# Kernel optimization log

Measured on AMD Instinct MI355X. Metric: run time of the kernel, lower is better.

## Reference

```python
import jax, jax.numpy as jnp
import numpy as np

GROUP = 128  # W4A16 quantization group size along the input (reduction) dim


def dequant(q, s, z):
    """Dequantize int4 weights. q: [out, in] ints in [0,16); s, z: [out, in//GROUP]."""
    out_f, in_f = q.shape
    g = in_f // GROUP
    qf = q.reshape(out_f, g, GROUP).astype(s.dtype)
    w = (qf - z[:, :, None]) * s[:, :, None]
    return w.reshape(out_f, in_f)


def setup_inputs() -> dict:
    key = jax.random.key(0)
    ks = jax.random.split(key, 11)
    H, I = 4096, 11008
    B, S = 4, 2048
    x = jax.random.normal(ks[0], (B, S, H), dtype=jnp.float32)
    qw_gate = jax.random.randint(ks[1], (I, H), 0, 16, dtype=jnp.int32)
    qw_up = jax.random.randint(ks[2], (I, H), 0, 16, dtype=jnp.int32)
    qw_down = jax.random.randint(ks[3], (H, I), 0, 16, dtype=jnp.int32)
    # scales small so dequantized weights have realistic magnitude; zeros in [0,16)
    s_gate = jax.random.uniform(ks[4], (I, H // GROUP), dtype=jnp.float32) * 0.01
    z_gate = jax.random.uniform(ks[5], (I, H // GROUP), dtype=jnp.float32) * 16.0
    s_up = jax.random.uniform(ks[6], (I, H // GROUP), dtype=jnp.float32) * 0.01
    z_up = jax.random.uniform(ks[7], (I, H // GROUP), dtype=jnp.float32) * 16.0
    s_down = jax.random.uniform(ks[8], (H, I // GROUP), dtype=jnp.float32) * 0.01
    z_down = jax.random.uniform(ks[9], (H, I // GROUP), dtype=jnp.float32) * 16.0
    return {
        "x": x,
        "qw_gate": qw_gate, "qw_up": qw_up, "qw_down": qw_down,
        "s_gate": s_gate, "z_gate": z_gate,
        "s_up": s_up, "z_up": z_up,
        "s_down": s_down, "z_down": z_down,
    }


def reference(x, qw_gate, qw_up, qw_down, s_gate, z_gate, s_up, z_up, s_down, z_down):
    # W4A16 SwiGLU MLP: down( silu(gate(x)) * up(x) )
    Wg = dequant(qw_gate, s_gate, z_gate)   # [I, H]
    Wu = dequant(qw_up, s_up, z_up)         # [I, H]
    Wd = dequant(qw_down, s_down, z_down)   # [H, I]
    g = jnp.einsum('bsh,ih->bsi', x, Wg)
    u = jnp.einsum('bsh,ih->bsi', x, Wu)
    h = jax.nn.silu(g) * u
    return jnp.einsum('bsi,hi->bsh', h, Wd)
```

## Files before the change

kernel.cpp:

```cpp
#include <hip/hip_runtime.h>
#include <hip/hip_fp16.h>

typedef __attribute__((ext_vector_type(8))) short s16x8;
typedef __attribute__((ext_vector_type(8))) _Float16 f16x8;
typedef __attribute__((ext_vector_type(4))) float f32x4;

__global__ void cvt_f32_to_f16_kernel(const float* __restrict__ in,
                                      __half* __restrict__ out, long n) {
  long i = (long)blockIdx.x * blockDim.x + threadIdx.x;
  long stride = (long)gridDim.x * blockDim.x;
  const float4* p4 = (const float4*)in;
  for (long j = i; j * 8 < n; j += stride) {
    float4 a = p4[j * 2];
    float4 b = p4[j * 2 + 1];
    union { s16x8 v; __half2 h2[4]; } w;
    w.h2[0] = __floats2half2_rn(a.x, a.y);
    w.h2[1] = __floats2half2_rn(a.z, a.w);
    w.h2[2] = __floats2half2_rn(b.x, b.y);
    w.h2[3] = __floats2half2_rn(b.z, b.w);
    *(s16x8*)(out + j * 8) = w.v;
  }
}

__global__ void pack_kernel(const int* __restrict__ q, uint32_t* __restrict__ p,
                            long n8) {
  long i = (long)blockIdx.x * blockDim.x + threadIdx.x;
  long stride = (long)gridDim.x * blockDim.x;
  for (; i < n8; i += stride) {
    int4 a = ((const int4*)q)[2 * i];
    int4 b = ((const int4*)q)[2 * i + 1];
    uint32_t w = (uint32_t)a.x | ((uint32_t)a.y << 4) | ((uint32_t)a.z << 8) |
                 ((uint32_t)a.w << 12) | ((uint32_t)b.x << 16) |
                 ((uint32_t)b.y << 20) | ((uint32_t)b.z << 24) |
                 ((uint32_t)b.w << 28);
    p[i] = w;
  }
}

__device__ __forceinline__ s16x8 dq_compute(int4 q0, int4 q1, float s, float z) {
  __half hs = __float2half(s);
  __half2 s2 = __halves2half2(hs, hs);
  __half hc = __float2half(-(64.f + z) * s);
  __half2 c2 = __halves2half2(hc, hc);
  uint32_t b0 = 0x54005400u + ((uint32_t)q0.x << 4) + ((uint32_t)q0.y << 20);
  uint32_t b1 = 0x54005400u + ((uint32_t)q0.z << 4) + ((uint32_t)q0.w << 20);
  uint32_t b2 = 0x54005400u + ((uint32_t)q1.x << 4) + ((uint32_t)q1.y << 20);
  uint32_t b3 = 0x54005400u + ((uint32_t)q1.z << 4) + ((uint32_t)q1.w << 20);
  union { s16x8 v; __half2 h2[4]; } w;
  w.h2[0] = __hfma2(*(__half2*)&b0, s2, c2);
  w.h2[1] = __hfma2(*(__half2*)&b1, s2, c2);
  w.h2[2] = __hfma2(*(__half2*)&b2, s2, c2);
  w.h2[3] = __hfma2(*(__half2*)&b3, s2, c2);
  return w.v;
}

__device__ __forceinline__ s16x8 dq8(uint32_t w, __half2 s2, __half2 c2) {
  union { s16x8 v; __half2 h2[4]; } r;
#pragma unroll
  for (int i = 0; i < 4; ++i) {
    uint32_t t = (w >> (8 * i)) & 0xFFu;
    uint32_t b = 0x54005400u + ((t & 15u) << 4) + ((t >> 4) << 20);
    r.h2[i] = __hfma2(*(__half2*)&b, s2, c2);
  }
  return r.v;
}

__device__ __forceinline__ int xcd_swz(int w0, int nwg) {
  const int q = nwg >> 3, r = nwg & 7;
  const int xcd = w0 & 7, idx = w0 >> 3;
  const int base = (xcd < r) ? xcd * (q + 1) : r * (q + 1) + (xcd - r) * q;
  return base + idx;
}

template <int PK>
__global__ __launch_bounds__(512, 2)
void gateup_kernel(const __half* __restrict__ Xh,
                   const int* __restrict__ Qg, const uint32_t* __restrict__ Pg,
                   const int* __restrict__ Qu, const uint32_t* __restrict__ Pu,
                   const float* __restrict__ Sg, const float* __restrict__ Zg,
                   const float* __restrict__ Su, const float* __restrict__ Zu,
                   __half* __restrict__ Pan, int mbs) {
  constexpr int H = 4096, I = 11008, G = 32;
  const int wg = xcd_swz(blockIdx.x, gridDim.x);
  const int mb = wg % mbs;
  const int nb = wg / mbs;
  const int m0 = mb * 256;
  const int n0 = nb * 128;
  const int tid = threadIdx.x;
  const int lane = tid & 63;
  const int wave = tid >> 6;
  const int wm = (wave >> 1) * 64, wn = (wave & 1) * 64;
  const int l15 = lane & 15, lq = lane >> 4;
  const int rsw = (l15 & 7) << 3;

  __shared__ __half As[2][256][64];
  __shared__ __half Bg[2][128][64];
  __shared__ __half Bu[2][128][64];

  f32x4 accg[4][4], accu[4][4];
#pragma unroll
  for (int i = 0; i < 4; ++i)
#pragma unroll
    for (int j = 0; j < 4; ++j) {
      accg[i][j] = {0.f, 0.f, 0.f, 0.f};
      accu[i][j] = {0.f, 0.f, 0.f, 0.f};
    }

  const int arowD = tid >> 3;
  const int acolD = (((tid & 7) ^ ((tid >> 3) & 7)) << 3);
  const int qrow = tid >> 2, qcol0 = (tid & 3) * 16, qsw = (qrow & 7) << 3;
  const int*      qPg = Qg + (size_t)(n0 + qrow) * H + qcol0;
  const int*      qPu = Qu + (size_t)(n0 + qrow) * H + qcol0;
  const uint32_t* pPg = Pg + (size_t)(n0 + qrow) * (H / 8) + (tid & 3) * 2;
  const uint32_t* pPu = Pu + (size_t)(n0 + qrow) * (H / 8) + (tid & 3) * 2;
  const float* sPg = Sg + (size_t)(n0 + qrow) * G;
  const float* zPg = Zg + (size_t)(n0 + qrow) * G;
  const float* sPu = Su + (size_t)(n0 + qrow) * G;
  const float* zPu = Zu + (size_t)(n0 + qrow) * G;

  int4 qG[4], qU[4];
  uint32_t wG0, wG1, wU0, wU1;
  float sG, zG, sU, zU;

#define STAGE_A(buf, kk)                                              \
  {                                                                   \
    const int _k = (kk);                                              \
    _Pragma("unroll")                                                 \
    for (int c = 0; c < 4; ++c) {                                     \
      const __half* src = Xh + (size_t)(m0 + c * 64 + arowD) * H + _k + acolD; \
      __half* dst = &As[buf][0][0] + (size_t)(c * 512 + tid) * 8;     \
      __builtin_amdgcn_global_load_lds((const __attribute__((address_space(1))) void*)src, \
                                       (__attribute__((address_space(3))) void*)dst, 16, 0, 0); \
    }                                                                 \
  }
#define LOAD_Q(kk)                                                    \
  {                                                                   \
    const int _k = (kk);                                              \
    if (PK) {                                                         \
      wG0 = pPg[_k >> 3]; wG1 = pPg[(_k >> 3) + 1];                   \
      wU0 = pPu[_k >> 3]; wU1 = pPu[(_k >> 3) + 1];                   \
    } else {                                                          \
      _Pragma("unroll")                                               \
      for (int i = 0; i < 4; ++i) qG[i] = ((const int4*)(qPg + _k))[i]; \
      _Pragma("unroll")                                               \
      for (int i = 0; i < 4; ++i) qU[i] = ((const int4*)(qPu + _k))[i]; \
    }                                                                 \
    sG = sPg[_k >> 7]; zG = zPg[_k >> 7];                             \
    sU = sPu[_k >> 7]; zU = zPu[_k >> 7];                             \
  }
#define WRITE_B(buf)                                                  \
  {                                                                   \
    if (PK) {                                                         \
      __half h1 = __float2half(sG);                                   \
      __half2 s2 = __halves2half2(h1, h1);                            \
      __half h2 = __float2half(-(64.f + zG) * sG);                    \
      __half2 c2 = __halves2half2(h2, h2);                            \
      *(s16x8*)&Bg[buf][qrow][(qcol0 + 0) ^ qsw] = dq8(wG0, s2, c2);  \
      *(s16x8*)&Bg[buf][qrow][(qcol0 + 8) ^ qsw] = dq8(wG1, s2, c2);  \
      __half h3 = __float2half(sU);                                   \
      __half2 s3 = __halves2half2(h3, h3);                            \
      __half h4 = __float2half(-(64.f + zU) * sU);                    \
      __half2 c3 = __halves2half2(h4, h4);                            \
      *(s16x8*)&Bu[buf][qrow][(qcol0 + 0) ^ qsw] = dq8(wU0, s3, c3);  \
      *(s16x8*)&Bu[buf][qrow][(qcol0 + 8) ^ qsw] = dq8(wU1, s3, c3);  \
    } else {                                                          \
      *(s16x8*)&Bg[buf][qrow][(qcol0 + 0) ^ qsw] = dq_compute(qG[0], qG[1], sG, zG); \
      *(s16x8*)&Bg[buf][qrow][(qcol0 + 8) ^ qsw] = dq_compute(qG[2], qG[3], sG, zG); \
      *(s16x8*)&Bu[buf][qrow][(qcol0 + 0) ^ qsw] = dq_compute(qU[0], qU[1], sU, zU); \
      *(s16x8*)&Bu[buf][qrow][(qcol0 + 8) ^ qsw] = dq_compute(qU[2], qU[3], sU, zU); \
    }                                                                 \
  }
#define MFMA_BUF(buf)                                                 \
  {                                                                   \
    __builtin_amdgcn_s_setprio(1);                                    \
    _Pragma("unroll")                                                 \
    for (int kk = 0; kk < 2; ++kk) {                                  \
      const int cbase = (kk * 32 + lq * 8) ^ rsw;                     \
      f16x8 af[4];                                                    \
      _Pragma("unroll")                                               \
      for (int i = 0; i < 4; ++i)                                     \
        af[i] = *(const f16x8*)&As[buf][wm + i * 16 + l15][cbase];    \
      _Pragma("unroll")                                               \
      for (int j = 0; j < 4; ++j) {                                   \
        f16x8 bg = *(const f16x8*)&Bg[buf][wn + j * 16 + l15][cbase]; \
        f16x8 bu = *(const f16x8*)&Bu[buf][wn + j * 16 + l15][cbase]; \
        _Pragma("unroll")                                             \
        for (int i = 0; i < 4; ++i) {                                 \
          accg[i][j] = __builtin_amdgcn_mfma_f32_16x16x32_f16(af[i], bg, accg[i][j], 0, 0, 0); \
          accu[i][j] = __builtin_amdgcn_mfma_f32_16x16x32_f16(af[i], bu, accu[i][j], 0, 0, 0); \
        }                                                             \
      }                                                               \
    }                                                                 \
    __builtin_amdgcn_s_setprio(0);                                    \
  }

  const int nt = H / 64;
  STAGE_A(0, 0)
  LOAD_Q(0)
  WRITE_B(0)
  __syncthreads();

  int p = 0;
  for (int t = 0; t < nt; ++t) {
    if (t + 1 < nt) {
      STAGE_A(p ^ 1, (t + 1) * 64)
      LOAD_Q((t + 1) * 64)
    }
    MFMA_BUF(p)
    if (t + 1 < nt) WRITE_B(p ^ 1)
    __syncthreads();
    p ^= 1;
  }
#undef STAGE_A
#undef LOAD_Q
#undef WRITE_B
#undef MFMA_BUF

#pragma unroll
  for (int i = 0; i < 4; ++i)
#pragma unroll
    for (int j = 0; j < 4; ++j)
#pragma unroll
      for (int r = 0; r < 4; ++r) {
        const int row = m0 + wm + i * 16 + lq * 4 + r;
        const int col = n0 + wn + j * 16 + l15;
        float g = accg[i][j][r];
        float u = accu[i][j][r];
        float hv = (g / (1.f + __expf(-g))) * u;
        Pan[(size_t)row * I + col] = __float2half(hv);
      }
}

template <int PK>
__global__ __launch_bounds__(512, 2)
void down_kernel(const __half* __restrict__ Hws,
                 const int* __restrict__ Qd, const uint32_t* __restrict__ QdP,
                 const float* __restrict__ Sd, const float* __restrict__ Zd,
                 float* __restrict__ Out, int mbs) {
  constexpr int K = 11008, N = 4096, G = 86;
  const int wg = xcd_swz(blockIdx.x, gridDim.x);
  const int mb = wg % mbs;
  const int nb = wg / mbs;
  const int m0 = mb * 256, n0 = nb * 128;
  const int tid = threadIdx.x;
  const int lane = tid & 63;
  const int wave = tid >> 6;
  const int wm = (wave >> 1) * 64, wn = (wave & 1) * 64;
  const int l15 = lane & 15, lq = lane >> 4;
  const int rsw = (l15 & 7) << 3;

  __shared__ __half As[2][256][64];
  __shared__ __half Bs[2][128][64];

  f32x4 acc[4][4];
#pragma unroll
  for (int i = 0; i < 4; ++i)
#pragma unroll
    for (int j = 0; j < 4; ++j) acc[i][j] = {0.f, 0.f, 0.f, 0.f};

  const int arowD = tid >> 3;
  const int acolD = (((tid & 7) ^ ((tid >> 3) & 7)) << 3);
  const int qrow = tid >> 2, qcol0 = (tid & 3) * 16, qsw = (qrow & 7) << 3;
  const int*      qP  = Qd  + (size_t)(n0 + qrow) * K + qcol0;
  const uint32_t* qPp = QdP + (size_t)(n0 + qrow) * (K / 8) + (tid & 3) * 2;
  const float* sP = Sd + (size_t)(n0 + qrow) * G;
  const float* zP = Zd + (size_t)(n0 + qrow) * G;

  int4 qA[4], qB[4];
  uint32_t wA0, wA1, wB0, wB1;
  float sA, zA, sB, zB;

#define STAGE_A(buf, kk)                                              \
  {                                                                   \
    const int _k = (kk);                                              \
    _Pragma("unroll")                                                 \
    for (int c = 0; c < 4; ++c) {                                     \
      const __half* src = Hws + (size_t)(m0 + c * 64 + arowD) * K + _k + acolD; \
      __half* dst = &As[buf][0][0] + (size_t)(c * 512 + tid) * 8;     \
      __builtin_amdgcn_global_load_lds((const __attribute__((address_space(1))) void*)src, \
                                       (__attribute__((address_space(3))) void*)dst, 16, 0, 0); \
    }                                                                 \
  }
#define LOAD_Q(set, kk)                                               \
  {                                                                   \
    const int _k = (kk);                                              \
    if (PK) {                                                         \
      w##set##0 = qPp[_k >> 3]; w##set##1 = qPp[(_k >> 3) + 1];       \
    } else {                                                          \
      _Pragma("unroll")                                               \
      for (int i = 0; i < 4; ++i) q##set[i] = ((const int4*)(qP + _k))[i]; \
    }                                                                 \
    s##set = sP[_k >> 7]; z##set = zP[_k >> 7];                       \
  }
#define WRITE_B(buf, set)                                             \
  {                                                                   \
    if (PK) {                                                         \
      __half hs = __float2half(s##set);                               \
      __half2 s2 = __halves2half2(hs, hs);                            \
      __half hc = __float2half(-(64.f + z##set) * s##set);            \
      __half2 c2 = __halves2half2(hc, hc);                            \
      *(s16x8*)&Bs[buf][qrow][(qcol0 + 0) ^ qsw] = dq8(w##set##0, s2, c2); \
      *(s16x8*)&Bs[buf][qrow][(qcol0 + 8) ^ qsw] = dq8(w##set##1, s2, c2); \
    } else {                                                          \
      *(s16x8*)&Bs[buf][qrow][(qcol0 + 0) ^ qsw] = dq_compute(q##set[0], q##set[1], s##set, z##set); \
      *(s16x8*)&Bs[buf][qrow][(qcol0 + 8) ^ qsw] = dq_compute(q##set[2], q##set[3], s##set, z##set); \
    }                                                                 \
  }
#define MFMA_BUF(buf)                                                 \
  {                                                                   \
    __builtin_amdgcn_s_setprio(1);                                    \
    _Pragma("unroll")                                                 \
    for (int kk = 0; kk < 2; ++kk) {                                  \
      const int cbase = (kk * 32 + lq * 8) ^ rsw;                     \
      f16x8 af[4];                                                    \
      _Pragma("unroll")                                               \
      for (int i = 0; i < 4; ++i)                                     \
        af[i] = *(const f16x8*)&As[buf][wm + i * 16 + l15][cbase];    \
      _Pragma("unroll")                                               \
      for (int j = 0; j < 4; ++j) {                                   \
        f16x8 bf = *(const f16x8*)&Bs[buf][wn + j * 16 + l15][cbase]; \
        _Pragma("unroll")                                             \
        for (int i = 0; i < 4; ++i)                                   \
          acc[i][j] = __builtin_amdgcn_mfma_f32_16x16x32_f16(af[i], bf, acc[i][j], 0, 0, 0); \
      }                                                               \
    }                                                                 \
    __builtin_amdgcn_s_setprio(0);                                    \
  }

  const int nt = K / 64;
  STAGE_A(0, 0)
  LOAD_Q(A, 0)
  LOAD_Q(B, 64)
  WRITE_B(0, A)
  __syncthreads();

  for (int t = 0; t < nt; t += 2) {
    if (t + 1 < nt) STAGE_A(1, (t + 1) * 64)
    if (t + 2 < nt) LOAD_Q(A, (t + 2) * 64)
    MFMA_BUF(0)
    if (t + 1 < nt) WRITE_B(1, B)
    __syncthreads();
    if (t + 2 < nt) STAGE_A(0, (t + 2) * 64)
    if (t + 3 < nt) LOAD_Q(B, (t + 3) * 64)
    MFMA_BUF(1)
    if (t + 2 < nt) WRITE_B(0, A)
    __syncthreads();
  }
#undef STAGE_A
#undef LOAD_Q
#undef WRITE_B
#undef MFMA_BUF

#pragma unroll
  for (int i = 0; i < 4; ++i)
#pragma unroll
    for (int j = 0; j < 4; ++j)
#pragma unroll
      for (int r = 0; r < 4; ++r) {
        const int row = m0 + wm + i * 16 + lq * 4 + r;
        const int col = n0 + wn + j * 16 + l15;
        Out[(size_t)row * N + col] = acc[i][j][r];
      }
}

extern "C" void kernel_launch(void* const* d_in, const int* in_sizes, int n_in,
                              void* d_out, int out_size, void* d_ws, size_t ws_size,
                              hipStream_t stream) {
  const float* x  = (const float*)d_in[0];
  const int* qg   = (const int*)d_in[1];
  const int* qu   = (const int*)d_in[2];
  const int* qd   = (const int*)d_in[3];
  const float* sg = (const float*)d_in[4];
  const float* zg = (const float*)d_in[5];
  const float* su = (const float*)d_in[6];
  const float* zu = (const float*)d_in[7];
  const float* sd = (const float*)d_in[8];
  const float* zd = (const float*)d_in[9];
  float* out = (float*)d_out;

  const int M = 8192, H = 4096, I = 11008;
  const long N8 = (long)I * H / 8;

  const int PD_MAX = 1375, PU_MAX = 4127;
  uint32_t* Pd = (uint32_t*)d_out;
  uint32_t* Pg = Pd + N8;
  uint32_t* Pu = Pg + N8;

  pack_kernel<<<2048, 256, 0, stream>>>(qd, Pd, N8);
  pack_kernel<<<2048, 256, 0, stream>>>(qg, Pg, N8);
  pack_kernel<<<2048, 256, 0, stream>>>(qu, Pu, N8);

  const size_t per_row = (size_t)(H + I) * 2;
  long mc = (long)(ws_size / per_row);
  mc &= ~255L;
  if (mc > M) mc = M;
  if (mc < 256) mc = 256;
  const int nch = (int)((M + mc - 1) / mc);
  int base = ((M / nch) / 256) * 256;
  if (base < 256) base = 256;
  int rem = M - base * nch;
  const int nplus = rem > 0 ? rem / 256 : 0;

  __half* wsx = (__half*)d_ws;
  const int McMax = base + (nplus > 0 ? 256 : 0);
  __half* wsh = (__half*)((char*)d_ws + (size_t)McMax * H * 2);

  int mbs_arr[64], mb_arr[64];
  {
    int mb = 0;
    for (int c = 0; c < nch; ++c) {
      int r = base + (c < nplus ? 256 : 0);
      mb_arr[c] = mb;
      mbs_arr[c] = r / 256;
      mb += r;
    }
  }

  int W = M;
  for (int c = nch - 1; c >= 0; --c) {
    const int mbase = mb_arr[c];
    const int mbs = mbs_arr[c];
    const int rows = mbs * 256;
    const bool gu_pk = (PU_MAX < W);
    const bool d_pk = (PD_MAX < W) && (PD_MAX < mbase);

    cvt_f32_to_f16_kernel<<<1024, 256, 0, stream>>>(
        x + (size_t)mbase * H, wsx, (long)rows * H);

    if (gu_pk)
      gateup_kernel<1><<<mbs * (I / 128), 512, 0, stream>>>(
          wsx, qg, Pg, qu, Pu, sg, zg, su, zu, wsh, mbs);
    else
      gateup_kernel<0><<<mbs * (I / 128), 512, 0, stream>>>(
          wsx, qg, Pg, qu, Pu, sg, zg, su, zu, wsh, mbs);

    if (d_pk)
      down_kernel<1><<<mbs * (H / 128), 512, 0, stream>>>(
          wsh, qd, Pd, sd, zd, out + (size_t)mbase * H, mbs);
    else
      down_kernel<0><<<mbs * (H / 128), 512, 0, stream>>>(
          wsh, qd, Pd, sd, zd, out + (size_t)mbase * H, mbs);

    W = mbase;
  }
}
```

Measured before the change: 3.383 ms.

## Fuse next-chunk activation conversion into down kernel and split gate/up packing

The fp32-to-fp16 conversion of the next row chunk's activations now runs inside the down-projection kernel. When that kernel has fewer than 256 GEMM blocks, extra blocks are launched to do the conversion, which removes a separate launch per chunk and lets the conversion overlap the down GEMM. Separately, the gate/up kernel now selects packed-int4 versus raw-int32 weight reads for gate and up independently, so gate can use packed weights once its pack region is no longer overwritten. This adds template variants and makes the down kernel write the shared activation workspace, which relies on gateup having finished reading it (guaranteed by stream order).

```diff
diff --git a/kernel.cpp b/kernel.cpp
--- a/kernel.cpp
+++ b/kernel.cpp
@@ -72,7 +72,7 @@
   return base + idx;
 }
 
-template <int PK>
+template <int PKG, int PKU>
 __global__ __launch_bounds__(512, 2)
 void gateup_kernel(const __half* __restrict__ Xh,
                    const int* __restrict__ Qg, const uint32_t* __restrict__ Pg,
@@ -136,12 +136,13 @@
 #define LOAD_Q(kk)                                                    \
   {                                                                   \
     const int _k = (kk);                                              \
-    if (PK) {                                                         \
-      wG0 = pPg[_k >> 3]; wG1 = pPg[(_k >> 3) + 1];                   \
-      wU0 = pPu[_k >> 3]; wU1 = pPu[(_k >> 3) + 1];                   \
-    } else {                                                          \
+    if (PKG) { wG0 = pPg[_k >> 3]; wG1 = pPg[(_k >> 3) + 1]; }        \
+    else {                                                            \
       _Pragma("unroll")                                               \
       for (int i = 0; i < 4; ++i) qG[i] = ((const int4*)(qPg + _k))[i]; \
+    }                                                                 \
+    if (PKU) { wU0 = pPu[_k >> 3]; wU1 = pPu[(_k >> 3) + 1]; }        \
+    else {                                                            \
       _Pragma("unroll")                                               \
       for (int i = 0; i < 4; ++i) qU[i] = ((const int4*)(qPu + _k))[i]; \
     }                                                                 \
@@ -150,13 +151,18 @@
   }
 #define WRITE_B(buf)                                                  \
   {                                                                   \
-    if (PK) {                                                         \
+    if (PKG) {                                                        \
       __half h1 = __float2half(sG);                                   \
       __half2 s2 = __halves2half2(h1, h1);                            \
       __half h2 = __float2half(-(64.f + zG) * sG);                    \
       __half2 c2 = __halves2half2(h2, h2);                            \
       *(s16x8*)&Bg[buf][qrow][(qcol0 + 0) ^ qsw] = dq8(wG0, s2, c2);  \
       *(s16x8*)&Bg[buf][qrow][(qcol0 + 8) ^ qsw] = dq8(wG1, s2, c2);  \
+    } else {                                                          \
+      *(s16x8*)&Bg[buf][qrow][(qcol0 + 0) ^ qsw] = dq_compute(qG[0], qG[1], sG, zG); \
+      *(s16x8*)&Bg[buf][qrow][(qcol0 + 8) ^ qsw] = dq_compute(qG[2], qG[3], sG, zG); \
+    }                                                                 \
+    if (PKU) {                                                        \
       __half h3 = __float2half(sU);                                   \
       __half2 s3 = __halves2half2(h3, h3);                            \
       __half h4 = __float2half(-(64.f + zU) * sU);                    \
@@ -164,8 +170,6 @@
       *(s16x8*)&Bu[buf][qrow][(qcol0 + 0) ^ qsw] = dq8(wU0, s3, c3);  \
       *(s16x8*)&Bu[buf][qrow][(qcol0 + 8) ^ qsw] = dq8(wU1, s3, c3);  \
     } else {                                                          \
-      *(s16x8*)&Bg[buf][qrow][(qcol0 + 0) ^ qsw] = dq_compute(qG[0], qG[1], sG, zG); \
-      *(s16x8*)&Bg[buf][qrow][(qcol0 + 8) ^ qsw] = dq_compute(qG[2], qG[3], sG, zG); \
       *(s16x8*)&Bu[buf][qrow][(qcol0 + 0) ^ qsw] = dq_compute(qU[0], qU[1], sU, zU); \
       *(s16x8*)&Bu[buf][qrow][(qcol0 + 8) ^ qsw] = dq_compute(qU[2], qU[3], sU, zU); \
     }                                                                 \
@@ -236,9 +240,32 @@
 void down_kernel(const __half* __restrict__ Hws,
                  const int* __restrict__ Qd, const uint32_t* __restrict__ QdP,
                  const float* __restrict__ Sd, const float* __restrict__ Zd,
-                 float* __restrict__ Out, int mbs) {
+                 float* __restrict__ Out, int mbs,
+                 const float* __restrict__ xnext, __half* __restrict__ wsx,
+                 long nunits) {
   constexpr int K = 11008, N = 4096, G = 86;
   const int wg = xcd_swz(blockIdx.x, gridDim.x);
+  const int gemmBlocks = mbs * 32;
+
+  if (wg >= gemmBlocks) {
+    const int cb = wg - gemmBlocks;
+    const int ncb = gridDim.x - gemmBlocks;
+    long i = (long)cb * 512 + threadIdx.x;
+    long stride = (long)ncb * 512;
+    const float4* p4 = (const float4*)xnext;
+    for (long j = i; j < nunits; j += stride) {
+      float4 a = p4[j * 2];
+      float4 b = p4[j * 2 + 1];
+      union { s16x8 v; __half2 h2[4]; } w;
+      w.h2[0] = __floats2half2_rn(a.x, a.y);
+      w.h2[1] = __floats2half2_rn(a.z, a.w);
+      w.h2[2] = __floats2half2_rn(b.x, b.y);
+      w.h2[3] = __floats2half2_rn(b.z, b.w);
+      *(s16x8*)(wsx + j * 8) = w.v;
+    }
+    return;
+  }
+
   const int mb = wg % mbs;
   const int nb = wg / mbs;
   const int m0 = mb * 256, n0 = nb * 128;
@@ -381,7 +408,7 @@
   const int M = 8192, H = 4096, I = 11008;
   const long N8 = (long)I * H / 8;
 
-  const int PD_MAX = 1375, PU_MAX = 4127;
+  const int PD_MAX = 1375, PG_MAX = 2751, PU_MAX = 4127;
   uint32_t* Pd = (uint32_t*)d_out;
   uint32_t* Pg = Pd + N8;
   uint32_t* Pu = Pg + N8;
@@ -416,30 +443,41 @@
     }
   }
 
+  {
+    const int c0 = nch - 1;
+    cvt_f32_to_f16_kernel<<<1024, 256, 0, stream>>>(
+        x + (size_t)mb_arr[c0] * H, wsx, (long)mbs_arr[c0] * 256 * H);
+  }
+
   int W = M;
   for (int c = nch - 1; c >= 0; --c) {
     const int mbase = mb_arr[c];
     const int mbs = mbs_arr[c];
-    const int rows = mbs * 256;
-    const bool gu_pk = (PU_MAX < W);
+    const bool g_pk = (PG_MAX < W);
+    const bool u_pk = (PU_MAX < W);
     const bool d_pk = (PD_MAX < W) && (PD_MAX < mbase);
 
-    cvt_f32_to_f16_kernel<<<1024, 256, 0, stream>>>(
-        x + (size_t)mbase * H, wsx, (long)rows * H);
-
-    if (gu_pk)
-      gateup_kernel<1><<<mbs * (I / 128), 512, 0, stream>>>(
+    if (u_pk)
+      gateup_kernel<1, 1><<<mbs * (I / 128), 512, 0, stream>>>(
+          wsx, qg, Pg, qu, Pu, sg, zg, su, zu, wsh, mbs);
+    else if (g_pk)
+      gateup_kernel<1, 0><<<mbs * (I / 128), 512, 0, stream>>>(
           wsx, qg, Pg, qu, Pu, sg, zg, su, zu, wsh, mbs);
     else
-      gateup_kernel<0><<<mbs * (I / 128), 512, 0, stream>>>(
+      gateup_kernel<0, 0><<<mbs * (I / 128), 512, 0, stream>>>(
           wsx, qg, Pg, qu, Pu, sg, zg, su, zu, wsh, mbs);
 
+    const float* xnext = (c > 0) ? x + (size_t)mb_arr[c - 1] * H : x;
+    const long nunits = (c > 0) ? (long)mbs_arr[c - 1] * 256 * H / 8 : 0;
+    int grid = mbs * 32;
+    if (grid < 256) grid = 256;
+
     if (d_pk)
-      down_kernel<1><<<mbs * (H / 128), 512, 0, stream>>>(
-          wsh, qd, Pd, sd, zd, out + (size_t)mbase * H, mbs);
+      down_kernel<1><<<grid, 512, 0, stream>>>(
+          wsh, qd, Pd, sd, zd, out + (size_t)mbase * H, mbs, xnext, wsx, nunits);
     else
-      down_kernel<0><<<mbs * (H / 128), 512, 0, stream>>>(
-          wsh, qd, Pd, sd, zd, out + (size_t)mbase * H, mbs);
+      down_kernel<0><<<grid, 512, 0, stream>>>(
+          wsh, qd, Pd, sd, zd, out + (size_t)mbase * H, mbs, xnext, wsx, nunits);
 
     W = mbase;
   }
```

After: 3.378 ms. No clear change (-0.1%).

## Stage fp16 activations in output buffer and split gate/up packed-weight flags

Applied to the files above, without the earlier changes.

The fp16 copy of x for each chunk now lives in the not-yet-written tail of the output buffer, so the workspace holds only the intermediate activations. This permits chunks of up to 2048 rows. Gate and up packed-weight usage are now decided independently, with separate thresholds tracking how much of the output buffer has been overwritten. The goal is to keep the 4-bit packed weights (which alias the output buffer) usable for longer and to cut traffic from the unpacked int32 weights. The cost is more intricate aliasing bookkeeping, where a mistake in the overwrite tracking could corrupt the packed weights.

```diff
diff --git a/kernel.cpp b/kernel.cpp
--- a/kernel.cpp
+++ b/kernel.cpp
@@ -72,7 +72,7 @@
   return base + idx;
 }
 
-template <int PK>
+template <int PKG, int PKU>
 __global__ __launch_bounds__(512, 2)
 void gateup_kernel(const __half* __restrict__ Xh,
                    const int* __restrict__ Qg, const uint32_t* __restrict__ Pg,
@@ -136,12 +136,13 @@
 #define LOAD_Q(kk)                                                    \
   {                                                                   \
     const int _k = (kk);                                              \
-    if (PK) {                                                         \
-      wG0 = pPg[_k >> 3]; wG1 = pPg[(_k >> 3) + 1];                   \
-      wU0 = pPu[_k >> 3]; wU1 = pPu[(_k >> 3) + 1];                   \
-    } else {                                                          \
+    if (PKG) { wG0 = pPg[_k >> 3]; wG1 = pPg[(_k >> 3) + 1]; }        \
+    else {                                                            \
       _Pragma("unroll")                                               \
       for (int i = 0; i < 4; ++i) qG[i] = ((const int4*)(qPg + _k))[i]; \
+    }                                                                 \
+    if (PKU) { wU0 = pPu[_k >> 3]; wU1 = pPu[(_k >> 3) + 1]; }        \
+    else {                                                            \
       _Pragma("unroll")                                               \
       for (int i = 0; i < 4; ++i) qU[i] = ((const int4*)(qPu + _k))[i]; \
     }                                                                 \
@@ -150,13 +151,18 @@
   }
 #define WRITE_B(buf)                                                  \
   {                                                                   \
-    if (PK) {                                                         \
+    if (PKG) {                                                        \
       __half h1 = __float2half(sG);                                   \
       __half2 s2 = __halves2half2(h1, h1);                            \
       __half h2 = __float2half(-(64.f + zG) * sG);                    \
       __half2 c2 = __halves2half2(h2, h2);                            \
       *(s16x8*)&Bg[buf][qrow][(qcol0 + 0) ^ qsw] = dq8(wG0, s2, c2);  \
       *(s16x8*)&Bg[buf][qrow][(qcol0 + 8) ^ qsw] = dq8(wG1, s2, c2);  \
+    } else {                                                          \
+      *(s16x8*)&Bg[buf][qrow][(qcol0 + 0) ^ qsw] = dq_compute(qG[0], qG[1], sG, zG); \
+      *(s16x8*)&Bg[buf][qrow][(qcol0 + 8) ^ qsw] = dq_compute(qG[2], qG[3], sG, zG); \
+    }                                                                 \
+    if (PKU) {                                                        \
       __half h3 = __float2half(sU);                                   \
       __half2 s3 = __halves2half2(h3, h3);                            \
       __half h4 = __float2half(-(64.f + zU) * sU);                    \
@@ -164,8 +170,6 @@
       *(s16x8*)&Bu[buf][qrow][(qcol0 + 0) ^ qsw] = dq8(wU0, s3, c3);  \
       *(s16x8*)&Bu[buf][qrow][(qcol0 + 8) ^ qsw] = dq8(wU1, s3, c3);  \
     } else {                                                          \
-      *(s16x8*)&Bg[buf][qrow][(qcol0 + 0) ^ qsw] = dq_compute(qG[0], qG[1], sG, zG); \
-      *(s16x8*)&Bg[buf][qrow][(qcol0 + 8) ^ qsw] = dq_compute(qG[2], qG[3], sG, zG); \
       *(s16x8*)&Bu[buf][qrow][(qcol0 + 0) ^ qsw] = dq_compute(qU[0], qU[1], sU, zU); \
       *(s16x8*)&Bu[buf][qrow][(qcol0 + 8) ^ qsw] = dq_compute(qU[2], qU[3], sU, zU); \
     }                                                                 \
@@ -381,7 +385,7 @@
   const int M = 8192, H = 4096, I = 11008;
   const long N8 = (long)I * H / 8;
 
-  const int PD_MAX = 1375, PU_MAX = 4127;
+  const int PD_MAX = 1375, PG_MAX = 2751, PU_MAX = 4127;
   uint32_t* Pd = (uint32_t*)d_out;
   uint32_t* Pg = Pd + N8;
   uint32_t* Pu = Pg + N8;
@@ -390,57 +394,55 @@
   pack_kernel<<<2048, 256, 0, stream>>>(qg, Pg, N8);
   pack_kernel<<<2048, 256, 0, stream>>>(qu, Pu, N8);
 
-  const size_t per_row = (size_t)(H + I) * 2;
-  long mc = (long)(ws_size / per_row);
+  long mc = (long)(ws_size / ((size_t)I * 2));
   mc &= ~255L;
-  if (mc > M) mc = M;
+  if (mc > 2048) mc = 2048;
   if (mc < 256) mc = 256;
-  const int nch = (int)((M + mc - 1) / mc);
-  int base = ((M / nch) / 256) * 256;
-  if (base < 256) base = 256;
-  int rem = M - base * nch;
-  const int nplus = rem > 0 ? rem / 256 : 0;
-
-  __half* wsx = (__half*)d_ws;
-  const int McMax = base + (nplus > 0 ? 256 : 0);
-  __half* wsh = (__half*)((char*)d_ws + (size_t)McMax * H * 2);
-
-  int mbs_arr[64], mb_arr[64];
-  {
-    int mb = 0;
-    for (int c = 0; c < nch; ++c) {
-      int r = base + (c < nplus ? 256 : 0);
-      mb_arr[c] = mb;
-      mbs_arr[c] = r / 256;
-      mb += r;
-    }
-  }
-
-  int W = M;
+  const int Mc = (int)mc;
+  __half* wsh = (__half*)d_ws;
+
+  int mb_arr[64], mbs_arr[64];
+  int nch = 0;
+  for (int mb = 0; mb < M; mb += Mc) {
+    mb_arr[nch] = mb;
+    mbs_arr[nch] = ((M - mb < Mc) ? (M - mb) : Mc) / 256;
+    ++nch;
+  }
+
+  int destr = M;
   for (int c = nch - 1; c >= 0; --c) {
     const int mbase = mb_arr[c];
     const int mbs = mbs_arr[c];
     const int rows = mbs * 256;
-    const bool gu_pk = (PU_MAX < W);
-    const bool d_pk = (PD_MAX < W) && (PD_MAX < mbase);
+    const int xrows = rows / 2;
+    const int wsxlo = mbase + rows - xrows;
+    __half* wsx = (__half*)(out + (size_t)wsxlo * H);
 
     cvt_f32_to_f16_kernel<<<1024, 256, 0, stream>>>(
         x + (size_t)mbase * H, wsx, (long)rows * H);
-
-    if (gu_pk)
-      gateup_kernel<1><<<mbs * (I / 128), 512, 0, stream>>>(
+    if (wsxlo < destr) destr = wsxlo;
+
+    const bool g_pk = (PG_MAX < destr);
+    const bool u_pk = (PU_MAX < destr);
+    const bool d_pk = (PD_MAX < destr) && (PD_MAX < mbase);
+
+    if (g_pk && u_pk)
+      gateup_kernel<1, 1><<<mbs * (I / 128), 512, 0, stream>>>(
+          wsx, qg, Pg, qu, Pu, sg, zg, su, zu, wsh, mbs);
+    else if (g_pk)
+      gateup_kernel<1, 0><<<mbs * (I / 128), 512, 0, stream>>>(
           wsx, qg, Pg, qu, Pu, sg, zg, su, zu, wsh, mbs);
     else
-      gateup_kernel<0><<<mbs * (I / 128), 512, 0, stream>>>(
+      gateup_kernel<0, 0><<<mbs * (I / 128), 512, 0, stream>>>(
           wsx, qg, Pg, qu, Pu, sg, zg, su, zu, wsh, mbs);
 
     if (d_pk)
-      down_kernel<1><<<mbs * (H / 128), 512, 0, stream>>>(
+      down_kernel<1><<<mbs * 32, 512, 0, stream>>>(
           wsh, qd, Pd, sd, zd, out + (size_t)mbase * H, mbs);
     else
-      down_kernel<0><<<mbs * (H / 128), 512, 0, stream>>>(
+      down_kernel<0><<<mbs * 32, 512, 0, stream>>>(
           wsh, qd, Pd, sd, zd, out + (size_t)mbase * H, mbs);
 
-    W = mbase;
-  }
-}
+    if (mbase < destr) destr = mbase;
+  }
+}
```

New measurement: 3.039 ms (median of 3 runs). 1.11x faster.
